# Kernel tuning notes

Hardware: AMD Instinct MI355X
Metric: run time of the kernel (lower is better)

Reference implementation:

```python
import jax, jax.numpy as jnp
import numpy as np


def setup_inputs() -> dict:
    key = jax.random.key(0)
    k1, k2 = jax.random.split(key)
    N, M, Q, D = 4096, 128, 64, 128
    a_embeddings = jax.random.normal(k1, (N, D), dtype=jnp.float32)
    b_embedding_sets = jax.random.normal(k2, (M, Q, D), dtype=jnp.float32)
    gaussian_variance = jnp.full((1,), 0.5, dtype=jnp.float32)  # nn.Parameter default
    return {
        "a_embeddings": a_embeddings,
        "b_embedding_sets": b_embedding_sets,
        "gaussian_variance": gaussian_variance,
    }


def reference(a_embeddings, b_embedding_sets, gaussian_variance):
    # Covariance = var * I, so inv(cov) = I / var and the Mahalanobis term is
    # ||a - mu||^2 / var. Expand the squared distance to avoid the NxMxQxD
    # broadcast intermediate the torch code materializes (same math).
    inv_var = 1.0 / gaussian_variance[0]
    a2 = jnp.sum(a_embeddings * a_embeddings, axis=-1)          # [N]
    b2 = jnp.sum(b_embedding_sets * b_embedding_sets, axis=-1)  # [M, Q]
    ab = jnp.einsum("nd,mqd->nmq", a_embeddings, b_embedding_sets)  # [N, M, Q]
    x2 = (a2[:, None, None] - 2.0 * ab + b2[None, :, :]) * inv_var  # [N, M, Q]
    densities = jnp.exp(-0.5 * x2)                  # [N, M, Q]
    dens_per_cluster = densities.sum(axis=2)        # [N, M]
    prob = dens_per_cluster / (dens_per_cluster.sum(axis=1, keepdims=True) + 1e-10)
    return prob
```

## Files before the change

kernel.cpp:

```cpp
#include <hip/hip_runtime.h>
#include <hip/hip_bf16.h>
#include <math.h>

#define NN 4096
#define MM 128
#define QQ 64
#define DD 128
#define CC (MM * QQ)

typedef short bf16x8 __attribute__((ext_vector_type(8)));
typedef float f32x4  __attribute__((ext_vector_type(4)));

static __device__ inline unsigned short f2bf(float f) {
    __hip_bfloat16 h = __float2bfloat16(f);
    return *reinterpret_cast<unsigned short*>(&h);
}

__global__ __launch_bounds__(256)
void prep_kernel(const float* __restrict__ A, const float* __restrict__ B,
                 unsigned short* __restrict__ Abf, unsigned short* __restrict__ Bbf,
                 float* __restrict__ a2, float* __restrict__ b2)
{
    const int row = blockIdx.x * 8 + (threadIdx.x >> 5);
    const int l32 = threadIdx.x & 31;
    const float* src;
    unsigned short* dst;
    float* nrm;
    if (row < NN) { src = A + (size_t)row * DD; dst = Abf + (size_t)row * DD; nrm = a2 + row; }
    else {
        int r = row - NN;
        src = B + (size_t)r * DD; dst = Bbf + (size_t)r * DD; nrm = b2 + r;
    }
    float4 v = ((const float4*)src)[l32];
    ushort4 u;
    u.x = f2bf(v.x); u.y = f2bf(v.y); u.z = f2bf(v.z); u.w = f2bf(v.w);
    ((ushort4*)dst)[l32] = u;
    float s = v.x * v.x + v.y * v.y + v.z * v.z + v.w * v.w;
    #pragma unroll
    for (int m = 16; m > 0; m >>= 1) s += __shfl_xor(s, m, 64);
    if (l32 == 0) *nrm = s;
}

__global__ __launch_bounds__(512, 4)
void kde_mfma_kernel(const unsigned short* __restrict__ Abf,
                     const unsigned short* __restrict__ Bbf,
                     const float* __restrict__ var,
                     const float* __restrict__ a2w,
                     const float* __restrict__ b2w,
                     float* __restrict__ dpc)
{
    __shared__ unsigned short Tile[256 * DD];
    __shared__ float a2s[128];
    __shared__ float b2s[128];
    __shared__ float red[8][32];

    const int lin = blockIdx.x;
    const int xcd = lin & 7;
    const int loc = lin >> 3;
    const int cb  = (xcd << 3) | (loc & 7);
    const int nb  = loc >> 3;
    const int n0  = nb * 128;
    const int c0  = cb * 128;

    const int t    = threadIdx.x;
    const int w    = t >> 6;
    const int lane = t & 63;

    const unsigned short* Ab = Abf + (size_t)n0 * DD;
    const unsigned short* Bb = Bbf + (size_t)c0 * DD;
    #pragma unroll
    for (int i = 0; i < 8; ++i) {
        const int slot = w * 512 + i * 64 + lane;
        const int r    = slot >> 4;
        const int c16  = slot & 15;
        const int scb  = c16 ^ (r & 7);
        const unsigned short* g = (r < 128) ? (Ab + r * DD + scb * 8)
                                            : (Bb + (r - 128) * DD + scb * 8);
        unsigned short* lbase = &Tile[(w * 512 + i * 64) * 8];
        __builtin_amdgcn_global_load_lds(
            (const __attribute__((address_space(1))) unsigned int*)g,
            (__attribute__((address_space(3))) unsigned int*)lbase,
            16, 0, 0);
    }
    if (t < 128)            a2s[t]       = a2w[n0 + t];
    else if (t < 256)       b2s[t - 128] = b2w[c0 + (t - 128)];
    __syncthreads();

    const int l15   = lane & 15;
    const int q     = lane >> 4;
    const int xr    = l15 & 7;
    const int rbase = (w & 3) * 32;
    const int cbase = (w >> 2) * 64;

    f32x4 acc[2][4] = {};
    #pragma unroll
    for (int ks = 0; ks < 4; ++ks) {
        const int off = ((ks * 4 + q) ^ xr) * 8;
        bf16x8 af[2], bf[4];
        #pragma unroll
        for (int i = 0; i < 2; ++i)
            af[i] = *(const bf16x8*)&Tile[(rbase + i * 16 + l15) * DD + off];
        #pragma unroll
        for (int j = 0; j < 4; ++j)
            bf[j] = *(const bf16x8*)&Tile[(128 + cbase + j * 16 + l15) * DD + off];
        #pragma unroll
        for (int i = 0; i < 2; ++i)
            #pragma unroll
            for (int j = 0; j < 4; ++j)
                acc[i][j] = __builtin_amdgcn_mfma_f32_16x16x32_bf16(
                                af[i], bf[j], acc[i][j], 0, 0, 0);
    }

    const float hinv = 0.5f / var[0];
    float rowsum[2][4];
    #pragma unroll
    for (int i = 0; i < 2; ++i) {
        #pragma unroll
        for (int reg = 0; reg < 4; ++reg) {
            const float a2 = a2s[rbase + i * 16 + q * 4 + reg];
            float p = 0.f;
            #pragma unroll
            for (int j = 0; j < 4; ++j) {
                const float b2 = b2s[cbase + j * 16 + l15];
                p += __expf((2.f * acc[i][j][reg] - a2 - b2) * hinv);
            }
            rowsum[i][reg] = p;
        }
    }
    #pragma unroll
    for (int mask = 1; mask < 16; mask <<= 1)
        #pragma unroll
        for (int i = 0; i < 2; ++i)
            #pragma unroll
            for (int reg = 0; reg < 4; ++reg)
                rowsum[i][reg] += __shfl_xor(rowsum[i][reg], mask, 64);

    if (l15 == 0) {
        #pragma unroll
        for (int i = 0; i < 2; ++i)
            #pragma unroll
            for (int reg = 0; reg < 4; ++reg)
                red[w][i * 16 + q * 4 + reg] = rowsum[i][reg];
    }
    const int m = (cb << 1) + (w >> 2);
    if (lane < 32)
        dpc[(size_t)m * NN + n0 + rbase + lane] = red[w][lane];
}

__global__ __launch_bounds__(1024)
void kde_norm_kernel(const float* __restrict__ dpc, float* __restrict__ out)
{
    __shared__ float tile[MM][65];
    __shared__ float rden[64];
    const int n0 = blockIdx.x * 64;
    const int t  = threadIdx.x;

    #pragma unroll
    for (int it = 0; it < 2; ++it) {
        const int m  = (t >> 4) + it * 64;
        const int nc = (t & 15) * 4;
        float4 v = *(const float4*)&dpc[(size_t)m * NN + n0 + nc];
        tile[m][nc]     = v.x;
        tile[m][nc + 1] = v.y;
        tile[m][nc + 2] = v.z;
        tile[m][nc + 3] = v.w;
    }
    __syncthreads();

    if (t < 64) {
        float s = 0.f;
        #pragma unroll 8
        for (int m = 0; m < MM; ++m) s += tile[m][t];
        rden[t] = 1.f / (s + 1e-10f);
    }
    __syncthreads();

    const int nloc = t >> 4;
    const int m0   = (t & 15) * 8;
    const float r  = rden[nloc];
    float4 o0, o1;
    o0.x = tile[m0][nloc] * r;     o0.y = tile[m0 + 1][nloc] * r;
    o0.z = tile[m0 + 2][nloc] * r; o0.w = tile[m0 + 3][nloc] * r;
    o1.x = tile[m0 + 4][nloc] * r; o1.y = tile[m0 + 5][nloc] * r;
    o1.z = tile[m0 + 6][nloc] * r; o1.w = tile[m0 + 7][nloc] * r;
    float* obase = &out[(size_t)(n0 + nloc) * MM + m0];
    *(float4*)obase       = o0;
    *(float4*)(obase + 4) = o1;
}

extern "C" void kernel_launch(void* const* d_in, const int* in_sizes, int n_in,
                              void* d_out, int out_size, void* d_ws, size_t ws_size,
                              hipStream_t stream) {
    const float* A   = (const float*)d_in[0];
    const float* B   = (const float*)d_in[1];
    const float* var = (const float*)d_in[2];
    float* out = (float*)d_out;

    unsigned short* Abf = (unsigned short*)d_ws;
    unsigned short* Bbf = Abf + (size_t)NN * DD;
    float* a2  = (float*)(Bbf + (size_t)CC * DD);
    float* b2  = a2 + NN;
    float* dpc = b2 + CC;

    prep_kernel<<<(NN + CC) / 8, 256, 0, stream>>>(A, B, Abf, Bbf, a2, b2);
    kde_mfma_kernel<<<2048, 512, 0, stream>>>(Abf, Bbf, var, a2, b2, dpc);
    kde_norm_kernel<<<NN / 64, 1024, 0, stream>>>(dpc, out);
}
```

Baseline: 85.90 us.

## Fuse prep, MFMA and normalize into one persistent kernel with grid barriers

Replaces three kernel launches with one persistent kernel of 512 blocks. The blocks synchronize through an atomic-counter grid barrier between the bf16 conversion, the MFMA/exp reduction and the normalization phases. Each block keeps its B tile resident in LDS and loops over four A tiles, so B reloads go down. This removes launch gaps and tail effects, but adds a memset, spin-wait barriers, a co-residency requirement of 512 blocks, and a serialized A-tile loop with no load/compute overlap.

Result: slower. 261.0 us (+203.8%).

```diff
diff --git a/kernel.cpp b/kernel.cpp
--- a/kernel.cpp
+++ b/kernel.cpp
@@ -16,176 +16,183 @@
     return *reinterpret_cast<unsigned short*>(&h);
 }
 
-__global__ __launch_bounds__(256)
-void prep_kernel(const float* __restrict__ A, const float* __restrict__ B,
-                 unsigned short* __restrict__ Abf, unsigned short* __restrict__ Bbf,
-                 float* __restrict__ a2, float* __restrict__ b2)
+static __device__ inline void grid_sync(unsigned int* cnt, unsigned int target) {
+    __syncthreads();
+    if (threadIdx.x == 0) {
+        __threadfence();
+        atomicAdd(cnt, 1u);
+        while (atomicAdd(cnt, 0u) < target) __builtin_amdgcn_s_sleep(1);
+    }
+    __syncthreads();
+    __threadfence();
+}
+
+__global__ __launch_bounds__(512, 4)
+void kde_mono_kernel(const float* __restrict__ A,
+                     const float* __restrict__ B,
+                     const float* __restrict__ var,
+                     unsigned short* __restrict__ Abf,
+                     unsigned short* __restrict__ Bbf,
+                     float* __restrict__ a2w, float* __restrict__ b2w,
+                     float* __restrict__ dpc,
+                     unsigned int* __restrict__ cnt,
+                     float* __restrict__ out)
 {
-    const int row = blockIdx.x * 8 + (threadIdx.x >> 5);
-    const int l32 = threadIdx.x & 31;
-    const float* src;
-    unsigned short* dst;
-    float* nrm;
-    if (row < NN) { src = A + (size_t)row * DD; dst = Abf + (size_t)row * DD; nrm = a2 + row; }
-    else {
-        int r = row - NN;
-        src = B + (size_t)r * DD; dst = Bbf + (size_t)r * DD; nrm = b2 + r;
-    }
-    float4 v = ((const float4*)src)[l32];
-    ushort4 u;
-    u.x = f2bf(v.x); u.y = f2bf(v.y); u.z = f2bf(v.z); u.w = f2bf(v.w);
-    ((ushort4*)dst)[l32] = u;
-    float s = v.x * v.x + v.y * v.y + v.z * v.z + v.w * v.w;
-    #pragma unroll
-    for (int m = 16; m > 0; m >>= 1) s += __shfl_xor(s, m, 64);
-    if (l32 == 0) *nrm = s;
-}
-
-__global__ __launch_bounds__(512, 4)
-void kde_mfma_kernel(const unsigned short* __restrict__ Abf,
-                     const unsigned short* __restrict__ Bbf,
-                     const float* __restrict__ var,
-                     const float* __restrict__ a2w,
-                     const float* __restrict__ b2w,
-                     float* __restrict__ dpc)
-{
-    __shared__ unsigned short Tile[256 * DD];
+    __shared__ unsigned short TA[128 * DD];
+    __shared__ unsigned short TB[128 * DD];
     __shared__ float a2s[128];
     __shared__ float b2s[128];
     __shared__ float red[8][32];
-
-    const int lin = blockIdx.x;
-    const int xcd = lin & 7;
-    const int loc = lin >> 3;
-    const int cb  = (xcd << 3) | (loc & 7);
-    const int nb  = loc >> 3;
-    const int n0  = nb * 128;
+    __shared__ float den3[8];
+
+    const int t = threadIdx.x;
+    const int b = blockIdx.x;
+
+    {
+        const int l32 = t & 31;
+        #pragma unroll
+        for (int it = 0; it < 2; ++it) {
+            const int lr = it * 16 + (t >> 5);
+            if (lr < 24) {
+                const int row = b * 24 + lr;
+                const float* src; unsigned short* dst; float* nrm;
+                if (row < NN) { src = A + (size_t)row * DD; dst = Abf + (size_t)row * DD; nrm = a2w + row; }
+                else { int r = row - NN; src = B + (size_t)r * DD; dst = Bbf + (size_t)r * DD; nrm = b2w + r; }
+                float4 v = ((const float4*)src)[l32];
+                ushort4 u;
+                u.x = f2bf(v.x); u.y = f2bf(v.y); u.z = f2bf(v.z); u.w = f2bf(v.w);
+                ((ushort4*)dst)[l32] = u;
+                float s = v.x * v.x + v.y * v.y + v.z * v.z + v.w * v.w;
+                #pragma unroll
+                for (int mk = 16; mk; mk >>= 1) s += __shfl_xor(s, mk, 64);
+                if (l32 == 0) *nrm = s;
+            }
+        }
+    }
+    grid_sync(cnt, 512);
+
+    const int w = t >> 6, lane = t & 63, l15 = lane & 15, q = lane >> 4;
+    const int xcd = b & 7, j = b >> 3;
+    const int cb  = (xcd << 3) | (j & 7);
+    const int nb0 = j >> 3;
     const int c0  = cb * 128;
-
-    const int t    = threadIdx.x;
-    const int w    = t >> 6;
-    const int lane = t & 63;
-
-    const unsigned short* Ab = Abf + (size_t)n0 * DD;
-    const unsigned short* Bb = Bbf + (size_t)c0 * DD;
-    #pragma unroll
-    for (int i = 0; i < 8; ++i) {
-        const int slot = w * 512 + i * 64 + lane;
-        const int r    = slot >> 4;
-        const int c16  = slot & 15;
-        const int scb  = c16 ^ (r & 7);
-        const unsigned short* g = (r < 128) ? (Ab + r * DD + scb * 8)
-                                            : (Bb + (r - 128) * DD + scb * 8);
-        unsigned short* lbase = &Tile[(w * 512 + i * 64) * 8];
-        __builtin_amdgcn_global_load_lds(
-            (const __attribute__((address_space(1))) unsigned int*)g,
-            (__attribute__((address_space(3))) unsigned int*)lbase,
-            16, 0, 0);
-    }
-    if (t < 128)            a2s[t]       = a2w[n0 + t];
-    else if (t < 256)       b2s[t - 128] = b2w[c0 + (t - 128)];
-    __syncthreads();
-
-    const int l15   = lane & 15;
-    const int q     = lane >> 4;
-    const int xr    = l15 & 7;
-    const int rbase = (w & 3) * 32;
-    const int cbase = (w >> 2) * 64;
-
-    f32x4 acc[2][4] = {};
-    #pragma unroll
-    for (int ks = 0; ks < 4; ++ks) {
-        const int off = ((ks * 4 + q) ^ xr) * 8;
-        bf16x8 af[2], bf[4];
-        #pragma unroll
-        for (int i = 0; i < 2; ++i)
-            af[i] = *(const bf16x8*)&Tile[(rbase + i * 16 + l15) * DD + off];
-        #pragma unroll
-        for (int j = 0; j < 4; ++j)
-            bf[j] = *(const bf16x8*)&Tile[(128 + cbase + j * 16 + l15) * DD + off];
-        #pragma unroll
-        for (int i = 0; i < 2; ++i)
-            #pragma unroll
-            for (int j = 0; j < 4; ++j)
-                acc[i][j] = __builtin_amdgcn_mfma_f32_16x16x32_bf16(
-                                af[i], bf[j], acc[i][j], 0, 0, 0);
-    }
-
     const float hinv = 0.5f / var[0];
-    float rowsum[2][4];
-    #pragma unroll
-    for (int i = 0; i < 2; ++i) {
-        #pragma unroll
-        for (int reg = 0; reg < 4; ++reg) {
-            const float a2 = a2s[rbase + i * 16 + q * 4 + reg];
-            float p = 0.f;
-            #pragma unroll
-            for (int j = 0; j < 4; ++j) {
-                const float b2 = b2s[cbase + j * 16 + l15];
-                p += __expf((2.f * acc[i][j][reg] - a2 - b2) * hinv);
+
+    {
+        const unsigned short* Bb = Bbf + (size_t)c0 * DD;
+        #pragma unroll
+        for (int i = 0; i < 4; ++i) {
+            const int slot = w * 256 + i * 64 + lane;
+            const int r = slot >> 4, c16 = slot & 15, scb = c16 ^ (r & 7);
+            const unsigned short* g = Bb + r * DD + scb * 8;
+            unsigned short* lbase = &TB[(w * 256 + i * 64) * 8];
+            __builtin_amdgcn_global_load_lds(
+                (const __attribute__((address_space(1))) unsigned int*)g,
+                (__attribute__((address_space(3))) unsigned int*)lbase, 16, 0, 0);
+        }
+        if (t >= 128 && t < 256) b2s[t - 128] = b2w[c0 + (t - 128)];
+    }
+
+    const int rbase = (w & 3) * 32, cbase = (w >> 2) * 64, xr = l15 & 7;
+    const int m = cb * 2 + (w >> 2);
+
+    for (int itn = 0; itn < 4; ++itn) {
+        const int n0 = (nb0 + itn * 8) * 128;
+        if (itn) __syncthreads();
+        {
+            const unsigned short* Ab = Abf + (size_t)n0 * DD;
+            #pragma unroll
+            for (int i = 0; i < 4; ++i) {
+                const int slot = w * 256 + i * 64 + lane;
+                const int r = slot >> 4, c16 = slot & 15, scb = c16 ^ (r & 7);
+                const unsigned short* g = Ab + r * DD + scb * 8;
+                unsigned short* lbase = &TA[(w * 256 + i * 64) * 8];
+                __builtin_amdgcn_global_load_lds(
+                    (const __attribute__((address_space(1))) unsigned int*)g,
+                    (__attribute__((address_space(3))) unsigned int*)lbase, 16, 0, 0);
             }
-            rowsum[i][reg] = p;
-        }
-    }
-    #pragma unroll
-    for (int mask = 1; mask < 16; mask <<= 1)
-        #pragma unroll
-        for (int i = 0; i < 2; ++i)
-            #pragma unroll
-            for (int reg = 0; reg < 4; ++reg)
-                rowsum[i][reg] += __shfl_xor(rowsum[i][reg], mask, 64);
-
-    if (l15 == 0) {
-        #pragma unroll
-        for (int i = 0; i < 2; ++i)
-            #pragma unroll
-            for (int reg = 0; reg < 4; ++reg)
-                red[w][i * 16 + q * 4 + reg] = rowsum[i][reg];
-    }
-    const int m = (cb << 1) + (w >> 2);
-    if (lane < 32)
-        dpc[(size_t)m * NN + n0 + rbase + lane] = red[w][lane];
-}
-
-__global__ __launch_bounds__(1024)
-void kde_norm_kernel(const float* __restrict__ dpc, float* __restrict__ out)
-{
-    __shared__ float tile[MM][65];
-    __shared__ float rden[64];
-    const int n0 = blockIdx.x * 64;
-    const int t  = threadIdx.x;
-
-    #pragma unroll
-    for (int it = 0; it < 2; ++it) {
-        const int m  = (t >> 4) + it * 64;
-        const int nc = (t & 15) * 4;
-        float4 v = *(const float4*)&dpc[(size_t)m * NN + n0 + nc];
-        tile[m][nc]     = v.x;
-        tile[m][nc + 1] = v.y;
-        tile[m][nc + 2] = v.z;
-        tile[m][nc + 3] = v.w;
-    }
-    __syncthreads();
-
-    if (t < 64) {
-        float s = 0.f;
-        #pragma unroll 8
-        for (int m = 0; m < MM; ++m) s += tile[m][t];
-        rden[t] = 1.f / (s + 1e-10f);
-    }
-    __syncthreads();
-
-    const int nloc = t >> 4;
-    const int m0   = (t & 15) * 8;
-    const float r  = rden[nloc];
-    float4 o0, o1;
-    o0.x = tile[m0][nloc] * r;     o0.y = tile[m0 + 1][nloc] * r;
-    o0.z = tile[m0 + 2][nloc] * r; o0.w = tile[m0 + 3][nloc] * r;
-    o1.x = tile[m0 + 4][nloc] * r; o1.y = tile[m0 + 5][nloc] * r;
-    o1.z = tile[m0 + 6][nloc] * r; o1.w = tile[m0 + 7][nloc] * r;
-    float* obase = &out[(size_t)(n0 + nloc) * MM + m0];
-    *(float4*)obase       = o0;
-    *(float4*)(obase + 4) = o1;
+            if (t < 128) a2s[t] = a2w[n0 + t];
+        }
+        __syncthreads();
+
+        f32x4 acc[2][4] = {};
+        #pragma unroll
+        for (int ks = 0; ks < 4; ++ks) {
+            const int off = ((ks * 4 + q) ^ xr) * 8;
+            bf16x8 af[2], bf[4];
+            #pragma unroll
+            for (int i = 0; i < 2; ++i)
+                af[i] = *(const bf16x8*)&TA[(rbase + i * 16 + l15) * DD + off];
+            #pragma unroll
+            for (int jj = 0; jj < 4; ++jj)
+                bf[jj] = *(const bf16x8*)&TB[(cbase + jj * 16 + l15) * DD + off];
+            #pragma unroll
+            for (int i = 0; i < 2; ++i)
+                #pragma unroll
+                for (int jj = 0; jj < 4; ++jj)
+                    acc[i][jj] = __builtin_amdgcn_mfma_f32_16x16x32_bf16(
+                                     af[i], bf[jj], acc[i][jj], 0, 0, 0);
+        }
+
+        float rowsum[2][4];
+        #pragma unroll
+        for (int i = 0; i < 2; ++i) {
+            #pragma unroll
+            for (int reg = 0; reg < 4; ++reg) {
+                const float a2 = a2s[rbase + i * 16 + q * 4 + reg];
+                float p = 0.f;
+                #pragma unroll
+                for (int jj = 0; jj < 4; ++jj) {
+                    const float b2 = b2s[cbase + jj * 16 + l15];
+                    p += __expf((2.f * acc[i][jj][reg] - a2 - b2) * hinv);
+                }
+                rowsum[i][reg] = p;
+            }
+        }
+        #pragma unroll
+        for (int mask = 1; mask < 16; mask <<= 1)
+            #pragma unroll
+            for (int i = 0; i < 2; ++i)
+                #pragma unroll
+                for (int reg = 0; reg < 4; ++reg)
+                    rowsum[i][reg] += __shfl_xor(rowsum[i][reg], mask, 64);
+
+        if (l15 == 0) {
+            #pragma unroll
+            for (int i = 0; i < 2; ++i)
+                #pragma unroll
+                for (int reg = 0; reg < 4; ++reg)
+                    red[w][i * 16 + q * 4 + reg] = rowsum[i][reg];
+        }
+        if (lane < 32)
+            dpc[(size_t)m * NN + n0 + rbase + lane] = red[w][lane];
+    }
+    grid_sync(cnt, 1024);
+
+    {
+        float* ftab = (float*)TA;
+        const int n0 = b * 8;
+        if (t < 256) {
+            const int mr = t >> 1, half = t & 1;
+            float4 v = *(const float4*)&dpc[(size_t)mr * NN + n0 + half * 4];
+            float* d = &ftab[mr * 9 + half * 4];
+            d[0] = v.x; d[1] = v.y; d[2] = v.z; d[3] = v.w;
+        }
+        __syncthreads();
+        if (t < 8) {
+            float s = 0.f;
+            #pragma unroll 8
+            for (int mr = 0; mr < MM; ++mr) s += ftab[mr * 9 + t];
+            den3[t] = 1.f / (s + 1e-10f);
+        }
+        __syncthreads();
+        const int nloc = t >> 6, m0 = (t & 63) * 2;
+        const float r = den3[nloc];
+        float2 o;
+        o.x = ftab[m0 * 9 + nloc] * r;
+        o.y = ftab[(m0 + 1) * 9 + nloc] * r;
+        *(float2*)&out[(size_t)(n0 + nloc) * MM + m0] = o;
+    }
 }
 
 extern "C" void kernel_launch(void* const* d_in, const int* in_sizes, int n_in,
@@ -196,13 +203,14 @@
     const float* var = (const float*)d_in[2];
     float* out = (float*)d_out;
 
-    unsigned short* Abf = (unsigned short*)d_ws;
-    unsigned short* Bbf = Abf + (size_t)NN * DD;
-    float* a2  = (float*)(Bbf + (size_t)CC * DD);
-    float* b2  = a2 + NN;
-    float* dpc = b2 + CC;
-
-    prep_kernel<<<(NN + CC) / 8, 256, 0, stream>>>(A, B, Abf, Bbf, a2, b2);
-    kde_mfma_kernel<<<2048, 512, 0, stream>>>(Abf, Bbf, var, a2, b2, dpc);
-    kde_norm_kernel<<<NN / 64, 1024, 0, stream>>>(dpc, out);
-}
+    char* ws = (char*)d_ws;
+    unsigned short* Abf = (unsigned short*)(ws);
+    unsigned short* Bbf = (unsigned short*)(ws + (1u << 20));
+    float* a2  = (float*)(ws + (3u << 20));
+    float* b2  = (float*)(ws + (3u << 20) + (1u << 16));
+    float* dpc = (float*)(ws + (4u << 20));
+    unsigned int* cnt = (unsigned int*)(ws + (8u << 20));
+
+    hipMemsetAsync(cnt, 0, sizeof(unsigned int), stream);
+    kde_mono_kernel<<<512, 512, 0, stream>>>(A, B, var, Abf, Bbf, a2, b2, dpc, cnt, out);
+}
```

## Fuse bf16 conversion and norm computation into density kernel, drop prep pass

Applied to the files above, without the earlier changes.

Removes the separate prep kernel. Each density block now loads its fp32 A and B tiles directly, converts them to bf16 by truncation into padded shared memory, and computes the squared norms in-block. This saves a kernel launch and the bf16/norm round trip through global memory. In exchange every block re-reads fp32 tiles (twice the bytes of bf16) and redoes the conversion redundantly across blocks. Truncation replaces round-to-nearest, which slightly changes precision.

Measured after the change: 105.1 us. 1.22x slower.

```diff
diff --git a/kernel.cpp b/kernel.cpp
--- a/kernel.cpp
+++ b/kernel.cpp
@@ -11,45 +11,21 @@
 typedef short bf16x8 __attribute__((ext_vector_type(8)));
 typedef float f32x4  __attribute__((ext_vector_type(4)));
 
-static __device__ inline unsigned short f2bf(float f) {
-    __hip_bfloat16 h = __float2bfloat16(f);
-    return *reinterpret_cast<unsigned short*>(&h);
-}
+#define LDA 136
 
-__global__ __launch_bounds__(256)
-void prep_kernel(const float* __restrict__ A, const float* __restrict__ B,
-                 unsigned short* __restrict__ Abf, unsigned short* __restrict__ Bbf,
-                 float* __restrict__ a2, float* __restrict__ b2)
-{
-    const int row = blockIdx.x * 8 + (threadIdx.x >> 5);
-    const int l32 = threadIdx.x & 31;
-    const float* src;
-    unsigned short* dst;
-    float* nrm;
-    if (row < NN) { src = A + (size_t)row * DD; dst = Abf + (size_t)row * DD; nrm = a2 + row; }
-    else {
-        int r = row - NN;
-        src = B + (size_t)r * DD; dst = Bbf + (size_t)r * DD; nrm = b2 + r;
-    }
-    float4 v = ((const float4*)src)[l32];
-    ushort4 u;
-    u.x = f2bf(v.x); u.y = f2bf(v.y); u.z = f2bf(v.z); u.w = f2bf(v.w);
-    ((ushort4*)dst)[l32] = u;
-    float s = v.x * v.x + v.y * v.y + v.z * v.z + v.w * v.w;
-    #pragma unroll
-    for (int m = 16; m > 0; m >>= 1) s += __shfl_xor(s, m, 64);
-    if (l32 == 0) *nrm = s;
+static __device__ inline unsigned short f2bf_trunc(float f) {
+    union { float f; unsigned int u; } c; c.f = f;
+    return (unsigned short)(c.u >> 16);
 }
 
 __global__ __launch_bounds__(512, 4)
-void kde_mfma_kernel(const unsigned short* __restrict__ Abf,
-                     const unsigned short* __restrict__ Bbf,
+void kde_dens_kernel(const float* __restrict__ A,
+                     const float* __restrict__ B,
                      const float* __restrict__ var,
-                     const float* __restrict__ a2w,
-                     const float* __restrict__ b2w,
                      float* __restrict__ dpc)
 {
-    __shared__ unsigned short Tile[256 * DD];
+    __shared__ unsigned short As[128 * LDA];
+    __shared__ unsigned short Bs[128 * LDA];
     __shared__ float a2s[128];
     __shared__ float b2s[128];
     __shared__ float red[8][32];
@@ -62,47 +38,52 @@
     const int n0  = nb * 128;
     const int c0  = cb * 128;
 
-    const int t    = threadIdx.x;
-    const int w    = t >> 6;
-    const int lane = t & 63;
+    const int t   = threadIdx.x;
+    const int l32 = t & 31;
+    const int rr  = t >> 5;
 
-    const unsigned short* Ab = Abf + (size_t)n0 * DD;
-    const unsigned short* Bb = Bbf + (size_t)c0 * DD;
     #pragma unroll
-    for (int i = 0; i < 8; ++i) {
-        const int slot = w * 512 + i * 64 + lane;
-        const int r    = slot >> 4;
-        const int c16  = slot & 15;
-        const int scb  = c16 ^ (r & 7);
-        const unsigned short* g = (r < 128) ? (Ab + r * DD + scb * 8)
-                                            : (Bb + (r - 128) * DD + scb * 8);
-        unsigned short* lbase = &Tile[(w * 512 + i * 64) * 8];
-        __builtin_amdgcn_global_load_lds(
-            (const __attribute__((address_space(1))) unsigned int*)g,
-            (__attribute__((address_space(3))) unsigned int*)lbase,
-            16, 0, 0);
+    for (int it = 0; it < 8; ++it) {
+        const int row = it * 16 + rr;
+        {
+            float4 v = *(const float4*)&A[(size_t)(n0 + row) * DD + l32 * 4];
+            ushort4 u;
+            u.x = f2bf_trunc(v.x); u.y = f2bf_trunc(v.y);
+            u.z = f2bf_trunc(v.z); u.w = f2bf_trunc(v.w);
+            *(ushort4*)&As[row * LDA + l32 * 4] = u;
+            float s = v.x * v.x + v.y * v.y + v.z * v.z + v.w * v.w;
+            #pragma unroll
+            for (int mk = 16; mk; mk >>= 1) s += __shfl_xor(s, mk, 64);
+            if (l32 == 0) a2s[row] = s;
+        }
+        {
+            float4 v = *(const float4*)&B[(size_t)(c0 + row) * DD + l32 * 4];
+            ushort4 u;
+            u.x = f2bf_trunc(v.x); u.y = f2bf_trunc(v.y);
+            u.z = f2bf_trunc(v.z); u.w = f2bf_trunc(v.w);
+            *(ushort4*)&Bs[row * LDA + l32 * 4] = u;
+            float s = v.x * v.x + v.y * v.y + v.z * v.z + v.w * v.w;
+            #pragma unroll
+            for (int mk = 16; mk; mk >>= 1) s += __shfl_xor(s, mk, 64);
+            if (l32 == 0) b2s[row] = s;
+        }
     }
-    if (t < 128)            a2s[t]       = a2w[n0 + t];
-    else if (t < 256)       b2s[t - 128] = b2w[c0 + (t - 128)];
     __syncthreads();
 
-    const int l15   = lane & 15;
-    const int q     = lane >> 4;
-    const int xr    = l15 & 7;
-    const int rbase = (w & 3) * 32;
-    const int cbase = (w >> 2) * 64;
+    const int w = t >> 6, lane = t & 63, l15 = lane & 15, q = lane >> 4;
+    const int rbase = (w & 3) * 32, cbase = (w >> 2) * 64;
 
     f32x4 acc[2][4] = {};
     #pragma unroll
     for (int ks = 0; ks < 4; ++ks) {
-        const int off = ((ks * 4 + q) ^ xr) * 8;
+        const int off = ks * 32 + q * 8;
         bf16x8 af[2], bf[4];
         #pragma unroll
         for (int i = 0; i < 2; ++i)
-            af[i] = *(const bf16x8*)&Tile[(rbase + i * 16 + l15) * DD + off];
+            af[i] = *(const bf16x8*)&As[(rbase + i * 16 + l15) * LDA + off];
         #pragma unroll
         for (int j = 0; j < 4; ++j)
-            bf[j] = *(const bf16x8*)&Tile[(128 + cbase + j * 16 + l15) * DD + off];
+            bf[j] = *(const bf16x8*)&Bs[(cbase + j * 16 + l15) * LDA + off];
         #pragma unroll
         for (int i = 0; i < 2; ++i)
             #pragma unroll
@@ -195,14 +176,8 @@
     const float* B   = (const float*)d_in[1];
     const float* var = (const float*)d_in[2];
     float* out = (float*)d_out;
+    float* dpc = (float*)d_ws;
 
-    unsigned short* Abf = (unsigned short*)d_ws;
-    unsigned short* Bbf = Abf + (size_t)NN * DD;
-    float* a2  = (float*)(Bbf + (size_t)CC * DD);
-    float* b2  = a2 + NN;
-    float* dpc = b2 + CC;
-
-    prep_kernel<<<(NN + CC) / 8, 256, 0, stream>>>(A, B, Abf, Bbf, a2, b2);
-    kde_mfma_kernel<<<2048, 512, 0, stream>>>(Abf, Bbf, var, a2, b2, dpc);
+    kde_dens_kernel<<<2048, 512, 0, stream>>>(A, B, var, dpc);
     kde_norm_kernel<<<NN / 64, 1024, 0, stream>>>(dpc, out);
 }
```

## Persistent density kernel reusing A tile with double-buffered B tiles

Applied to the files above, without the earlier changes.

The density kernel now launches 256 blocks of 1024 threads instead of 2048 blocks of 512. Each block keeps its 128-row A tile in LDS and loops over 8 B column tiles. The next B tile is prefetched into a second LDS buffer while MFMA and exp run on the current one. This cuts redundant A loads and launch/prologue overhead, at the cost of fewer blocks in flight (256 on a 256-CU part), a barrier on every iteration, and a larger LDS footprint per block.

Measured after the change: 87.84 us. 2.2% more time.

```diff
diff --git a/kernel.cpp b/kernel.cpp
--- a/kernel.cpp
+++ b/kernel.cpp
@@ -10,6 +10,9 @@
 
 typedef short bf16x8 __attribute__((ext_vector_type(8)));
 typedef float f32x4  __attribute__((ext_vector_type(4)));
+
+#define AS1 __attribute__((address_space(1)))
+#define AS3 __attribute__((address_space(3)))
 
 static __device__ inline unsigned short f2bf(float f) {
     __hip_bfloat16 h = __float2bfloat16(f);
@@ -41,110 +44,115 @@
     if (l32 == 0) *nrm = s;
 }
 
-__global__ __launch_bounds__(512, 4)
-void kde_mfma_kernel(const unsigned short* __restrict__ Abf,
+__global__ __launch_bounds__(1024, 4)
+void kde_dens_kernel(const unsigned short* __restrict__ Abf,
                      const unsigned short* __restrict__ Bbf,
                      const float* __restrict__ var,
                      const float* __restrict__ a2w,
                      const float* __restrict__ b2w,
                      float* __restrict__ dpc)
 {
-    __shared__ unsigned short Tile[256 * DD];
+    __shared__ unsigned short As[128 * DD];
+    __shared__ unsigned short Bs[2][128 * DD];
     __shared__ float a2s[128];
-    __shared__ float b2s[128];
-    __shared__ float red[8][32];
-
-    const int lin = blockIdx.x;
-    const int xcd = lin & 7;
-    const int loc = lin >> 3;
-    const int cb  = (xcd << 3) | (loc & 7);
-    const int nb  = loc >> 3;
+    __shared__ float b2s[2][128];
+
+    const int b   = blockIdx.x;
+    const int xcd = b & 7;
+    const int nb  = b >> 3;
     const int n0  = nb * 128;
-    const int c0  = cb * 128;
-
-    const int t    = threadIdx.x;
-    const int w    = t >> 6;
-    const int lane = t & 63;
-
-    const unsigned short* Ab = Abf + (size_t)n0 * DD;
-    const unsigned short* Bb = Bbf + (size_t)c0 * DD;
-    #pragma unroll
-    for (int i = 0; i < 8; ++i) {
-        const int slot = w * 512 + i * 64 + lane;
-        const int r    = slot >> 4;
-        const int c16  = slot & 15;
-        const int scb  = c16 ^ (r & 7);
-        const unsigned short* g = (r < 128) ? (Ab + r * DD + scb * 8)
-                                            : (Bb + (r - 128) * DD + scb * 8);
-        unsigned short* lbase = &Tile[(w * 512 + i * 64) * 8];
-        __builtin_amdgcn_global_load_lds(
-            (const __attribute__((address_space(1))) unsigned int*)g,
-            (__attribute__((address_space(3))) unsigned int*)lbase,
-            16, 0, 0);
-    }
-    if (t < 128)            a2s[t]       = a2w[n0 + t];
-    else if (t < 256)       b2s[t - 128] = b2w[c0 + (t - 128)];
+
+    const int t = threadIdx.x, w = t >> 6, lane = t & 63;
+
+    {
+        const unsigned short* Ab = Abf + (size_t)n0 * DD;
+        #pragma unroll
+        for (int i = 0; i < 2; ++i) {
+            const int slot = w * 128 + i * 64 + lane;
+            const int r = slot >> 4, c16 = slot & 15, scb = c16 ^ (r & 7);
+            __builtin_amdgcn_global_load_lds(
+                (const AS1 unsigned int*)(Ab + r * DD + scb * 8),
+                (AS3 unsigned int*)&As[(w * 128 + i * 64) * 8], 16, 0, 0);
+        }
+        if (t < 128) a2s[t] = a2w[n0 + t];
+    }
+    {
+        const int cb = (xcd << 3) | (nb & 7);
+        const unsigned short* Bb = Bbf + (size_t)cb * 128 * DD;
+        #pragma unroll
+        for (int i = 0; i < 2; ++i) {
+            const int slot = w * 128 + i * 64 + lane;
+            const int r = slot >> 4, c16 = slot & 15, scb = c16 ^ (r & 7);
+            __builtin_amdgcn_global_load_lds(
+                (const AS1 unsigned int*)(Bb + r * DD + scb * 8),
+                (AS3 unsigned int*)&Bs[0][(w * 128 + i * 64) * 8], 16, 0, 0);
+        }
+        if (t >= 128 && t < 256) b2s[0][t - 128] = b2w[cb * 128 + (t - 128)];
+    }
     __syncthreads();
 
-    const int l15   = lane & 15;
-    const int q     = lane >> 4;
-    const int xr    = l15 & 7;
-    const int rbase = (w & 3) * 32;
-    const int cbase = (w >> 2) * 64;
-
-    f32x4 acc[2][4] = {};
-    #pragma unroll
-    for (int ks = 0; ks < 4; ++ks) {
-        const int off = ((ks * 4 + q) ^ xr) * 8;
-        bf16x8 af[2], bf[4];
-        #pragma unroll
-        for (int i = 0; i < 2; ++i)
-            af[i] = *(const bf16x8*)&Tile[(rbase + i * 16 + l15) * DD + off];
-        #pragma unroll
-        for (int j = 0; j < 4; ++j)
-            bf[j] = *(const bf16x8*)&Tile[(128 + cbase + j * 16 + l15) * DD + off];
-        #pragma unroll
-        for (int i = 0; i < 2; ++i)
-            #pragma unroll
-            for (int j = 0; j < 4; ++j)
-                acc[i][j] = __builtin_amdgcn_mfma_f32_16x16x32_bf16(
-                                af[i], bf[j], acc[i][j], 0, 0, 0);
-    }
-
+    const int l15 = lane & 15, q = lane >> 4, xr = l15 & 7;
+    const int rbase = (w & 7) * 16;
+    const int chalf = w >> 3;
+    const int cbase = chalf * 64;
     const float hinv = 0.5f / var[0];
-    float rowsum[2][4];
-    #pragma unroll
-    for (int i = 0; i < 2; ++i) {
+
+    for (int it = 0; it < 8; ++it) {
+        const int cur = it & 1;
+        const int cb  = (xcd << 3) | ((nb + it) & 7);
+
+        if (it < 7) {
+            const int cbn = (xcd << 3) | ((nb + it + 1) & 7);
+            const unsigned short* Bb = Bbf + (size_t)cbn * 128 * DD;
+            #pragma unroll
+            for (int i = 0; i < 2; ++i) {
+                const int slot = w * 128 + i * 64 + lane;
+                const int r = slot >> 4, c16 = slot & 15, scb = c16 ^ (r & 7);
+                __builtin_amdgcn_global_load_lds(
+                    (const AS1 unsigned int*)(Bb + r * DD + scb * 8),
+                    (AS3 unsigned int*)&Bs[1 - cur][(w * 128 + i * 64) * 8], 16, 0, 0);
+            }
+            if (t >= 128 && t < 256) b2s[1 - cur][t - 128] = b2w[cbn * 128 + (t - 128)];
+        }
+
+        f32x4 acc[4] = {};
+        #pragma unroll
+        for (int ks = 0; ks < 4; ++ks) {
+            const int off = ((ks * 4 + q) ^ xr) * 8;
+            const bf16x8 af = *(const bf16x8*)&As[(rbase + l15) * DD + off];
+            #pragma unroll
+            for (int j = 0; j < 4; ++j) {
+                const bf16x8 bf = *(const bf16x8*)&Bs[cur][(cbase + j * 16 + l15) * DD + off];
+                acc[j] = __builtin_amdgcn_mfma_f32_16x16x32_bf16(af, bf, acc[j], 0, 0, 0);
+            }
+        }
+
+        float rowsum[4];
         #pragma unroll
         for (int reg = 0; reg < 4; ++reg) {
-            const float a2 = a2s[rbase + i * 16 + q * 4 + reg];
+            const float a2 = a2s[rbase + q * 4 + reg];
             float p = 0.f;
             #pragma unroll
             for (int j = 0; j < 4; ++j) {
-                const float b2 = b2s[cbase + j * 16 + l15];
-                p += __expf((2.f * acc[i][j][reg] - a2 - b2) * hinv);
+                const float b2 = b2s[cur][cbase + j * 16 + l15];
+                p += __expf((2.f * acc[j][reg] - a2 - b2) * hinv);
             }
-            rowsum[i][reg] = p;
-        }
-    }
-    #pragma unroll
-    for (int mask = 1; mask < 16; mask <<= 1)
-        #pragma unroll
-        for (int i = 0; i < 2; ++i)
+            rowsum[reg] = p;
+        }
+        #pragma unroll
+        for (int mask = 1; mask < 16; mask <<= 1)
             #pragma unroll
             for (int reg = 0; reg < 4; ++reg)
-                rowsum[i][reg] += __shfl_xor(rowsum[i][reg], mask, 64);
-
-    if (l15 == 0) {
-        #pragma unroll
-        for (int i = 0; i < 2; ++i)
-            #pragma unroll
-            for (int reg = 0; reg < 4; ++reg)
-                red[w][i * 16 + q * 4 + reg] = rowsum[i][reg];
-    }
-    const int m = (cb << 1) + (w >> 2);
-    if (lane < 32)
-        dpc[(size_t)m * NN + n0 + rbase + lane] = red[w][lane];
+                rowsum[reg] += __shfl_xor(rowsum[reg], mask, 64);
+
+        if (l15 == 0) {
+            const int m = cb * 2 + chalf;
+            f32x4 o = {rowsum[0], rowsum[1], rowsum[2], rowsum[3]};
+            *(f32x4*)&dpc[(size_t)m * NN + n0 + rbase + q * 4] = o;
+        }
+
+        __syncthreads();
+    }
 }
 
 __global__ __launch_bounds__(1024)
@@ -203,6 +211,6 @@
     float* dpc = b2 + CC;
 
     prep_kernel<<<(NN + CC) / 8, 256, 0, stream>>>(A, B, Abf, Bbf, a2, b2);
-    kde_mfma_kernel<<<2048, 512, 0, stream>>>(Abf, Bbf, var, a2, b2, dpc);
+    kde_dens_kernel<<<256, 1024, 0, stream>>>(Abf, Bbf, var, a2, b2, dpc);
     kde_norm_kernel<<<NN / 64, 1024, 0, stream>>>(dpc, out);
 }
```
